# Kernel tuning notes

Hardware: AMD Instinct MI355X
Metric: run time of the kernel (lower is better)

The kernel has to match this reference:

```python
import jax, jax.numpy as jnp
import numpy as np

MARGIN = 0.2
LAMBDA_CLS = 1.0
LAMBDA_TRIPLET = 1.0
EPS = 1e-6  # matches torch pairwise_distance eps inside TripletMarginLoss
B, D, C = 8192, 192, 1024


def setup_inputs() -> dict:
    key = jax.random.key(0)
    k1, k2, k3 = jax.random.split(key, 3)
    embeddings = jax.random.normal(k1, (B, D), dtype=jnp.float32)
    logits = jax.random.normal(k2, (B, C), dtype=jnp.float32)
    targets = jax.random.randint(k3, (B,), 0, C, dtype=jnp.int64)
    return {"embeddings": embeddings, "logits": logits, "targets": targets}


def reference(embeddings, logits, targets):
    # ---- classification loss: mean cross entropy ----
    logp = jax.nn.log_softmax(logits, axis=-1)
    cls_loss = -jnp.mean(jnp.take_along_axis(logp, targets[:, None], axis=1))

    # ---- vectorized hard triplet mining (mining='hard'), on detached embeddings ----
    e = jax.lax.stop_gradient(embeddings)
    sq = jnp.sum(e * e, axis=1)                       # [B]
    d2 = sq[:, None] + sq[None, :] - 2.0 * (e @ e.T)  # [B, B]
    dist = jnp.sqrt(jnp.maximum(d2, 0.0))

    same = targets[:, None] == targets[None, :]       # [B, B]
    eye = jnp.eye(targets.shape[0], dtype=bool)
    pos_mask = same & ~eye
    neg_mask = ~same
    valid = pos_mask.any(axis=1) & neg_mask.any(axis=1)

    # hard positive: farthest same-speaker; hard negative: closest other-speaker
    pos_idx = jnp.argmax(jnp.where(pos_mask, dist, -jnp.inf), axis=1)
    neg_idx = jnp.argmin(jnp.where(neg_mask, dist, jnp.inf), axis=1)

    # ---- triplet margin loss on live embeddings ----
    a = embeddings
    p = embeddings[pos_idx]
    n = embeddings[neg_idx]
    d_ap = jnp.linalg.norm(a - p + EPS, axis=1)
    d_an = jnp.linalg.norm(a - n + EPS, axis=1)
    per_triplet = jnp.maximum(d_ap - d_an + MARGIN, 0.0)

    w = valid.astype(per_triplet.dtype)
    cnt = jnp.sum(w)
    trip_loss = jnp.where(cnt > 0, jnp.sum(per_triplet * w) / jnp.maximum(cnt, 1.0), 0.0)

    return LAMBDA_CLS * cls_loss + LAMBDA_TRIPLET * trip_loss
```

## Files before the change

kernel.cpp:

```cpp
#include <hip/hip_runtime.h>
#include <math.h>

#define B_N    8192
#define D_DIM  192
#define C_CLS  1024
#define MARGIN 0.2f
#define EPS_T  1e-6f

#define TI     128
#define TJ     128
#define JSPLIT 8
#define JLEN   (B_N / JSPLIT)
#define LDB    200

typedef __attribute__((ext_vector_type(8))) short v8s;
typedef __attribute__((ext_vector_type(4))) float v4f;
typedef __attribute__((ext_vector_type(4))) int   v4i;

__device__ __forceinline__ unsigned fkey(float f) {
  unsigned u = __float_as_uint(f);
  return (u & 0x80000000u) ? ~u : (u | 0x80000000u);
}

__device__ __forceinline__ unsigned short to_bf(float x) {
  unsigned u = __float_as_uint(x);
  u += 0x7fffu + ((u >> 16) & 1u);
  return (unsigned short)(u >> 16);
}

__global__ __launch_bounds__(256) void cvt_kernel(const float* __restrict__ e,
                                                  unsigned short* __restrict__ ebf) {
  int t = blockIdx.x * 256 + threadIdx.x;
  float4 v = ((const float4*)e)[t];
  ushort4 o;
  o.x = to_bf(v.x); o.y = to_bf(v.y); o.z = to_bf(v.z); o.w = to_bf(v.w);
  ((ushort4*)ebf)[t] = o;
}

__global__ __launch_bounds__(256) void sq_kernel(const float* __restrict__ e,
                                                 float* __restrict__ sq) {
  int w = threadIdx.x >> 6, lane = threadIdx.x & 63;
  int row = blockIdx.x * 4 + w;
  const float* p = e + (size_t)row * D_DIM;
  float v0 = p[lane], v1 = p[lane + 64], v2 = p[lane + 128];
  float s = v0 * v0 + v1 * v1 + v2 * v2;
  #pragma unroll
  for (int off = 32; off; off >>= 1) s += __shfl_xor(s, off);
  if (lane == 0) sq[row] = s;
}

__global__ __launch_bounds__(256, 2) void mine_kernel(
    const unsigned short* __restrict__ ebf, const int* __restrict__ tgt,
    const float* __restrict__ sq,
    unsigned long long* __restrict__ posw, unsigned long long* __restrict__ negw) {
  __shared__ unsigned short lds_b[TJ * LDB];
  __shared__ int   lds_t[TJ];
  __shared__ float lds_s[TJ];

  const int tid  = threadIdx.x;
  const int w    = tid >> 6;
  const int lane = tid & 63;
  const int ln15 = lane & 15;
  const int quad = lane >> 4;
  const int i0      = blockIdx.x * TI;
  const int j_begin = blockIdx.y * JLEN;

  int my_t[2][4];
  {
    const int base = i0 + w * 32 + quad * 4;
    v4i t0 = *(const v4i*)&tgt[base];
    v4i t1 = *(const v4i*)&tgt[base + 16];
    my_t[0][0] = t0.x; my_t[0][1] = t0.y; my_t[0][2] = t0.z; my_t[0][3] = t0.w;
    my_t[1][0] = t1.x; my_t[1][1] = t1.y; my_t[1][2] = t1.z; my_t[1][3] = t1.w;
  }

  v8s afrag[2][6];
  #pragma unroll
  for (int ra = 0; ra < 2; ++ra) {
    const unsigned short* ap =
        ebf + (size_t)(i0 + w * 32 + ra * 16 + ln15) * D_DIM + quad * 8;
    #pragma unroll
    for (int ks = 0; ks < 6; ++ks)
      afrag[ra][ks] = *(const v8s*)(ap + ks * 32);
  }

  float    pv[2][4], nv[2][4];
  unsigned pi_[2][4], ni_[2][4];
  #pragma unroll
  for (int ra = 0; ra < 2; ++ra)
    #pragma unroll
    for (int r = 0; r < 4; ++r) {
      pv[ra][r] = -3.4e38f; nv[ra][r] = 3.4e38f;
      pi_[ra][r] = 0u; ni_[ra][r] = 0xFFFFFFFFu;
    }

  for (int j0 = j_begin; j0 < j_begin + JLEN; j0 += TJ) {
    __syncthreads();
    #pragma unroll
    for (int t = 0; t < 12; ++t) {
      int c = t * 256 + tid;
      int row = c / 24;
      int off = c - row * 24;
      v8s v = *(const v8s*)(ebf + (size_t)(j0 + row) * D_DIM + off * 8);
      *(v8s*)&lds_b[row * LDB + off * 8] = v;
    }
    if (tid < TJ) { lds_t[tid] = tgt[j0 + tid]; lds_s[tid] = sq[j0 + tid]; }
    __syncthreads();

    v4f acc[2][8];
    #pragma unroll
    for (int ra = 0; ra < 2; ++ra)
      #pragma unroll
      for (int tb = 0; tb < 8; ++tb)
        acc[ra][tb] = (v4f){0.f, 0.f, 0.f, 0.f};

    #pragma unroll
    for (int ks = 0; ks < 6; ++ks) {
      v8s bfr[8];
      #pragma unroll
      for (int tb = 0; tb < 8; ++tb)
        bfr[tb] = *(const v8s*)&lds_b[(tb * 16 + ln15) * LDB + ks * 32 + quad * 8];
      #pragma unroll
      for (int ra = 0; ra < 2; ++ra)
        #pragma unroll
        for (int tb = 0; tb < 8; ++tb)
          acc[ra][tb] = __builtin_amdgcn_mfma_f32_16x16x32_bf16(
              afrag[ra][ks], bfr[tb], acc[ra][tb], 0, 0, 0);
    }

    #pragma unroll
    for (int tb = 0; tb < 8; ++tb) {
      int jl = tb * 16 + ln15;
      int jg = j0 + jl;
      int tc = lds_t[jl];
      float s = lds_s[jl];
      #pragma unroll
      for (int ra = 0; ra < 2; ++ra)
        #pragma unroll
        for (int r = 0; r < 4; ++r) {
          float val  = fmaf(acc[ra][tb][r], -2.0f, s);
          bool  same = (tc == my_t[ra][r]);
          float vp = same ? val : -3.4e38f;
          float vn = same ? 3.4e38f : val;
          if (vp > pv[ra][r]) { pv[ra][r] = vp; pi_[ra][r] = (unsigned)jg; }
          if (vn < nv[ra][r]) { nv[ra][r] = vn; ni_[ra][r] = (unsigned)jg; }
        }
    }
  }

  #pragma unroll
  for (int ra = 0; ra < 2; ++ra)
    #pragma unroll
    for (int r = 0; r < 4; ++r) {
      unsigned long long pk =
          ((unsigned long long)fkey(pv[ra][r]) << 32) |
          (unsigned long long)(unsigned)(~pi_[ra][r]);
      unsigned long long nk =
          ((unsigned long long)fkey(nv[ra][r]) << 32) |
          (unsigned long long)ni_[ra][r];
      #pragma unroll
      for (int off = 1; off < 16; off <<= 1) {
        unsigned long long po = __shfl_xor(pk, off);
        unsigned long long no = __shfl_xor(nk, off);
        pk = pk > po ? pk : po;
        nk = nk < no ? nk : no;
      }
      if (ln15 == 0) {
        int row = i0 + w * 32 + ra * 16 + quad * 4 + r;
        atomicMax(&posw[row], pk);
        atomicMin(&negw[row], nk);
      }
    }
}

__global__ __launch_bounds__(1024) void ce_kernel(const float* __restrict__ logits,
                                                  const int* __restrict__ tgt,
                                                  float* __restrict__ accum) {
  __shared__ float part[16];
  int w = threadIdx.x >> 6, lane = threadIdx.x & 63;
  int row = blockIdx.x * 16 + w;
  const float* p = logits + (size_t)row * C_CLS;
  float4 x[4];
  #pragma unroll
  for (int t = 0; t < 4; ++t) x[t] = *(const float4*)(p + lane * 4 + 256 * t);
  float m = -3.4e38f;
  #pragma unroll
  for (int t = 0; t < 4; ++t)
    m = fmaxf(m, fmaxf(fmaxf(x[t].x, x[t].y), fmaxf(x[t].z, x[t].w)));
  #pragma unroll
  for (int off = 32; off; off >>= 1) m = fmaxf(m, __shfl_xor(m, off));
  float s = 0.f;
  #pragma unroll
  for (int t = 0; t < 4; ++t)
    s += __expf(x[t].x - m) + __expf(x[t].y - m) +
         __expf(x[t].z - m) + __expf(x[t].w - m);
  #pragma unroll
  for (int off = 32; off; off >>= 1) s += __shfl_xor(s, off);
  if (lane == 0) part[w] = m + __logf(s) - p[tgt[row]];
  __syncthreads();
  if (threadIdx.x == 0) {
    float t = 0.f;
    #pragma unroll
    for (int i = 0; i < 16; ++i) t += part[i];
    atomicAdd(accum, t);
  }
}

__global__ __launch_bounds__(1024) void trip_kernel(
    const float* __restrict__ e,
    const unsigned long long* __restrict__ posw,
    const unsigned long long* __restrict__ negw,
    float* __restrict__ accum) {
  __shared__ float ssum[16];
  __shared__ float scnt[16];
  int w = threadIdx.x >> 6, lane = threadIdx.x & 63;
  int i = blockIdx.x * 16 + w;
  unsigned long long pp = posw[i], np = negw[i];
  unsigned pidx = ~(unsigned)pp;
  unsigned nidx = (unsigned)np;
  float res = 0.f, c = 0.f;
  if (pp != 0ULL && np != ~0ULL && pidx != (unsigned)i) {
    const float* pa = e + (size_t)i * D_DIM;
    const float* pb = e + (size_t)pidx * D_DIM;
    const float* pc = e + (size_t)nidx * D_DIM;
    float dap = 0.f, dan = 0.f;
    #pragma unroll
    for (int t = 0; t < 3; ++t) {
      int k = lane + 64 * t;
      float av = pa[k];
      float d1 = av - pb[k] + EPS_T;
      float d2 = av - pc[k] + EPS_T;
      dap += d1 * d1;
      dan += d2 * d2;
    }
    #pragma unroll
    for (int off = 32; off; off >>= 1) {
      dap += __shfl_xor(dap, off);
      dan += __shfl_xor(dan, off);
    }
    res = fmaxf(sqrtf(dap) - sqrtf(dan) + MARGIN, 0.f);
    c = 1.f;
  }
  if (lane == 0) { ssum[w] = res; scnt[w] = c; }
  __syncthreads();
  if (threadIdx.x == 0) {
    float a = 0.f, b = 0.f;
    #pragma unroll
    for (int k = 0; k < 16; ++k) { a += ssum[k]; b += scnt[k]; }
    atomicAdd(&accum[1], a);
    atomicAdd(&accum[2], b);
  }
}

__global__ void fin_kernel(const float* __restrict__ accum, float* __restrict__ out) {
  float cls = accum[0] / (float)B_N;
  float ts = accum[1], tc = accum[2];
  float trip = (tc > 0.f) ? ts / fmaxf(tc, 1.f) : 0.f;
  out[0] = cls + trip;
}

extern "C" void kernel_launch(void* const* d_in, const int* in_sizes, int n_in,
                              void* d_out, int out_size, void* d_ws, size_t ws_size,
                              hipStream_t stream) {
  const float* emb    = (const float*)d_in[0];
  const float* logits = (const float*)d_in[1];
  const int*   tgt    = (const int*)d_in[2];
  float* out = (float*)d_out;

  char* ws = (char*)d_ws;
  unsigned short* ebf = (unsigned short*)ws;
  unsigned long long* posw = (unsigned long long*)(ws + 3145728);
  unsigned long long* negw = (unsigned long long*)(ws + 3145728 + 65536);
  float* sq    = (float*)(ws + 3145728 + 131072);
  float* accum = (float*)(ws + 3145728 + 163840);

  hipMemsetAsync(posw, 0, 65536, stream);
  hipMemsetAsync(negw, 0xFF, 65536, stream);
  hipMemsetAsync(accum, 0, 16, stream);

  cvt_kernel<<<1536, 256, 0, stream>>>(emb, ebf);
  sq_kernel<<<2048, 256, 0, stream>>>(emb, sq);
  mine_kernel<<<dim3(B_N / TI, JSPLIT), 256, 0, stream>>>(ebf, tgt, sq, posw, negw);
  ce_kernel<<<512, 1024, 0, stream>>>(logits, tgt, accum);
  trip_kernel<<<512, 1024, 0, stream>>>(emb, posw, negw, accum);
  fin_kernel<<<1, 1, 0, stream>>>(accum, out);
}
```

Before: 174.6 us.

## Fuse prep, CE and finalize kernels; switch mining to 32x32 MFMA tiles

```diff
diff --git a/kernel.cpp b/kernel.cpp
--- a/kernel.cpp
+++ b/kernel.cpp
@@ -13,9 +13,8 @@
 #define JLEN   (B_N / JSPLIT)
 #define LDB    200
 
-typedef __attribute__((ext_vector_type(8))) short v8s;
-typedef __attribute__((ext_vector_type(4))) float v4f;
-typedef __attribute__((ext_vector_type(4))) int   v4i;
+typedef short v8s  __attribute__((ext_vector_type(8)));
+typedef float v16f __attribute__((ext_vector_type(16)));
 
 __device__ __forceinline__ unsigned fkey(float f) {
   unsigned u = __float_as_uint(f);
@@ -28,189 +27,180 @@
   return (unsigned short)(u >> 16);
 }
 
-__global__ __launch_bounds__(256) void cvt_kernel(const float* __restrict__ e,
-                                                  unsigned short* __restrict__ ebf) {
-  int t = blockIdx.x * 256 + threadIdx.x;
-  float4 v = ((const float4*)e)[t];
-  ushort4 o;
-  o.x = to_bf(v.x); o.y = to_bf(v.y); o.z = to_bf(v.z); o.w = to_bf(v.w);
-  ((ushort4*)ebf)[t] = o;
-}
-
-__global__ __launch_bounds__(256) void sq_kernel(const float* __restrict__ e,
-                                                 float* __restrict__ sq) {
+__global__ __launch_bounds__(256) void prep_kernel(
+    const float* __restrict__ e, unsigned short* __restrict__ ebf,
+    float* __restrict__ sq,
+    unsigned long long* __restrict__ posw, unsigned long long* __restrict__ negw,
+    float* __restrict__ accum) {
   int w = threadIdx.x >> 6, lane = threadIdx.x & 63;
   int row = blockIdx.x * 4 + w;
   const float* p = e + (size_t)row * D_DIM;
   float v0 = p[lane], v1 = p[lane + 64], v2 = p[lane + 128];
+  unsigned short* q = ebf + (size_t)row * D_DIM;
+  q[lane] = to_bf(v0); q[lane + 64] = to_bf(v1); q[lane + 128] = to_bf(v2);
   float s = v0 * v0 + v1 * v1 + v2 * v2;
   #pragma unroll
   for (int off = 32; off; off >>= 1) s += __shfl_xor(s, off);
   if (lane == 0) sq[row] = s;
+  int b = blockIdx.x;
+  if (b < 32)       posw[b * 256 + threadIdx.x] = 0ULL;
+  else if (b < 64)  negw[(b - 32) * 256 + threadIdx.x] = ~0ULL;
+  else if (b == 64 && threadIdx.x < 4) ((unsigned*)accum)[threadIdx.x] = 0u;
 }
 
 __global__ __launch_bounds__(256, 2) void mine_kernel(
     const unsigned short* __restrict__ ebf, const int* __restrict__ tgt,
-    const float* __restrict__ sq,
-    unsigned long long* __restrict__ posw, unsigned long long* __restrict__ negw) {
+    const float* __restrict__ sq, const float* __restrict__ logits,
+    unsigned long long* __restrict__ posw, unsigned long long* __restrict__ negw,
+    float* __restrict__ accum) {
   __shared__ unsigned short lds_b[TJ * LDB];
   __shared__ int   lds_t[TJ];
   __shared__ float lds_s[TJ];
+  __shared__ float ce_part[4];
 
   const int tid  = threadIdx.x;
   const int w    = tid >> 6;
   const int lane = tid & 63;
-  const int ln15 = lane & 15;
-  const int quad = lane >> 4;
-  const int i0      = blockIdx.x * TI;
-  const int j_begin = blockIdx.y * JLEN;
-
-  int my_t[2][4];
+  const int n5   = lane & 31;
+  const int h    = lane >> 5;
+  const int wj   = w & 1;
+  const int wi   = w >> 1;
+  const int i0 = blockIdx.x * TI;
+  const int jb = blockIdx.y * JLEN;
+
   {
-    const int base = i0 + w * 32 + quad * 4;
-    v4i t0 = *(const v4i*)&tgt[base];
-    v4i t1 = *(const v4i*)&tgt[base + 16];
-    my_t[0][0] = t0.x; my_t[0][1] = t0.y; my_t[0][2] = t0.z; my_t[0][3] = t0.w;
-    my_t[1][0] = t1.x; my_t[1][1] = t1.y; my_t[1][2] = t1.z; my_t[1][3] = t1.w;
-  }
-
-  v8s afrag[2][6];
-  #pragma unroll
-  for (int ra = 0; ra < 2; ++ra) {
-    const unsigned short* ap =
-        ebf + (size_t)(i0 + w * 32 + ra * 16 + ln15) * D_DIM + quad * 8;
-    #pragma unroll
-    for (int ks = 0; ks < 6; ++ks)
-      afrag[ra][ks] = *(const v8s*)(ap + ks * 32);
-  }
-
-  float    pv[2][4], nv[2][4];
-  unsigned pi_[2][4], ni_[2][4];
-  #pragma unroll
-  for (int ra = 0; ra < 2; ++ra)
-    #pragma unroll
-    for (int r = 0; r < 4; ++r) {
-      pv[ra][r] = -3.4e38f; nv[ra][r] = 3.4e38f;
-      pi_[ra][r] = 0u; ni_[ra][r] = 0xFFFFFFFFu;
-    }
-
-  for (int j0 = j_begin; j0 < j_begin + JLEN; j0 += TJ) {
-    __syncthreads();
+    const unsigned short* src = ebf + (size_t)i0 * D_DIM;
     #pragma unroll
     for (int t = 0; t < 12; ++t) {
       int c = t * 256 + tid;
       int row = c / 24;
       int off = c - row * 24;
-      v8s v = *(const v8s*)(ebf + (size_t)(j0 + row) * D_DIM + off * 8);
-      *(v8s*)&lds_b[row * LDB + off * 8] = v;
+      *(v8s*)&lds_b[row * LDB + off * 8] = *(const v8s*)(src + (size_t)row * D_DIM + off * 8);
+    }
+  }
+  __syncthreads();
+  v8s bfrag[2][12];
+  #pragma unroll
+  for (int tb = 0; tb < 2; ++tb)
+    #pragma unroll
+    for (int kc = 0; kc < 12; ++kc)
+      bfrag[tb][kc] = *(const v8s*)&lds_b[(wi * 64 + tb * 32 + n5) * LDB + kc * 16 + h * 8];
+
+  int my_t[2];
+  #pragma unroll
+  for (int tb = 0; tb < 2; ++tb) my_t[tb] = tgt[i0 + wi * 64 + tb * 32 + n5];
+
+  float    pv[2] = {-3.4e38f, -3.4e38f}, nv[2] = {3.4e38f, 3.4e38f};
+  unsigned pi_[2] = {0u, 0u}, ni_[2] = {0xFFFFFFFFu, 0xFFFFFFFFu};
+
+  for (int j0 = jb; j0 < jb + JLEN; j0 += TJ) {
+    __syncthreads();
+    #pragma unroll
+    for (int t = 0; t < 12; ++t) {
+      int c = t * 256 + tid;
+      int row = c / 24;
+      int off = c - row * 24;
+      *(v8s*)&lds_b[row * LDB + off * 8] =
+          *(const v8s*)(ebf + (size_t)(j0 + row) * D_DIM + off * 8);
     }
     if (tid < TJ) { lds_t[tid] = tgt[j0 + tid]; lds_s[tid] = sq[j0 + tid]; }
     __syncthreads();
 
-    v4f acc[2][8];
-    #pragma unroll
-    for (int ra = 0; ra < 2; ++ra)
+    v16f acc[2][2];
+    #pragma unroll
+    for (int ta = 0; ta < 2; ++ta)
       #pragma unroll
-      for (int tb = 0; tb < 8; ++tb)
-        acc[ra][tb] = (v4f){0.f, 0.f, 0.f, 0.f};
-
-    #pragma unroll
-    for (int ks = 0; ks < 6; ++ks) {
-      v8s bfr[8];
+      for (int tb = 0; tb < 2; ++tb)
+        #pragma unroll
+        for (int r = 0; r < 16; ++r) acc[ta][tb][r] = 0.f;
+
+    #pragma unroll
+    for (int kc = 0; kc < 12; ++kc) {
+      v8s afr0 = *(const v8s*)&lds_b[(wj * 64 +  0 + n5) * LDB + kc * 16 + h * 8];
+      v8s afr1 = *(const v8s*)&lds_b[(wj * 64 + 32 + n5) * LDB + kc * 16 + h * 8];
+      acc[0][0] = __builtin_amdgcn_mfma_f32_32x32x16_bf16(afr0, bfrag[0][kc], acc[0][0], 0, 0, 0);
+      acc[0][1] = __builtin_amdgcn_mfma_f32_32x32x16_bf16(afr0, bfrag[1][kc], acc[0][1], 0, 0, 0);
+      acc[1][0] = __builtin_amdgcn_mfma_f32_32x32x16_bf16(afr1, bfrag[0][kc], acc[1][0], 0, 0, 0);
+      acc[1][1] = __builtin_amdgcn_mfma_f32_32x32x16_bf16(afr1, bfrag[1][kc], acc[1][1], 0, 0, 0);
+    }
+
+    #pragma unroll
+    for (int ta = 0; ta < 2; ++ta)
       #pragma unroll
-      for (int tb = 0; tb < 8; ++tb)
-        bfr[tb] = *(const v8s*)&lds_b[(tb * 16 + ln15) * LDB + ks * 32 + quad * 8];
-      #pragma unroll
-      for (int ra = 0; ra < 2; ++ra)
+      for (int p = 0; p < 4; ++p) {
+        int jb4 = wj * 64 + ta * 32 + p * 8 + h * 4;
+        float4 s4 = *(const float4*)&lds_s[jb4];
+        int4   t4 = *(const int4*)&lds_t[jb4];
         #pragma unroll
-        for (int tb = 0; tb < 8; ++tb)
-          acc[ra][tb] = __builtin_amdgcn_mfma_f32_16x16x32_bf16(
-              afrag[ra][ks], bfr[tb], acc[ra][tb], 0, 0, 0);
-    }
-
-    #pragma unroll
-    for (int tb = 0; tb < 8; ++tb) {
-      int jl = tb * 16 + ln15;
-      int jg = j0 + jl;
-      int tc = lds_t[jl];
-      float s = lds_s[jl];
-      #pragma unroll
-      for (int ra = 0; ra < 2; ++ra)
-        #pragma unroll
-        for (int r = 0; r < 4; ++r) {
-          float val  = fmaf(acc[ra][tb][r], -2.0f, s);
-          bool  same = (tc == my_t[ra][r]);
-          float vp = same ? val : -3.4e38f;
-          float vn = same ? 3.4e38f : val;
-          if (vp > pv[ra][r]) { pv[ra][r] = vp; pi_[ra][r] = (unsigned)jg; }
-          if (vn < nv[ra][r]) { nv[ra][r] = vn; ni_[ra][r] = (unsigned)jg; }
+        for (int q = 0; q < 3 + 1; ++q) {
+          float sv = (q == 0) ? s4.x : (q == 1) ? s4.y : (q == 2) ? s4.z : s4.w;
+          int   tv = (q == 0) ? t4.x : (q == 1) ? t4.y : (q == 2) ? t4.z : t4.w;
+          unsigned jg = (unsigned)(j0 + jb4 + q);
+          #pragma unroll
+          for (int tb = 0; tb < 2; ++tb) {
+            float val = fmaf(acc[ta][tb][p * 4 + q], -2.0f, sv);
+            bool same = (tv == my_t[tb]);
+            float vp = same ? val : -3.4e38f;
+            float vn = same ? 3.4e38f : val;
+            if (vp > pv[tb]) { pv[tb] = vp; pi_[tb] = jg; }
+            if (vn < nv[tb]) { nv[tb] = vn; ni_[tb] = jg; }
+          }
         }
-    }
-  }
-
-  #pragma unroll
-  for (int ra = 0; ra < 2; ++ra)
-    #pragma unroll
-    for (int r = 0; r < 4; ++r) {
-      unsigned long long pk =
-          ((unsigned long long)fkey(pv[ra][r]) << 32) |
-          (unsigned long long)(unsigned)(~pi_[ra][r]);
-      unsigned long long nk =
-          ((unsigned long long)fkey(nv[ra][r]) << 32) |
-          (unsigned long long)ni_[ra][r];
-      #pragma unroll
-      for (int off = 1; off < 16; off <<= 1) {
-        unsigned long long po = __shfl_xor(pk, off);
-        unsigned long long no = __shfl_xor(nk, off);
-        pk = pk > po ? pk : po;
-        nk = nk < no ? nk : no;
       }
-      if (ln15 == 0) {
-        int row = i0 + w * 32 + ra * 16 + quad * 4 + r;
-        atomicMax(&posw[row], pk);
-        atomicMin(&negw[row], nk);
-      }
-    }
-}
-
-__global__ __launch_bounds__(1024) void ce_kernel(const float* __restrict__ logits,
-                                                  const int* __restrict__ tgt,
-                                                  float* __restrict__ accum) {
-  __shared__ float part[16];
-  int w = threadIdx.x >> 6, lane = threadIdx.x & 63;
-  int row = blockIdx.x * 16 + w;
-  const float* p = logits + (size_t)row * C_CLS;
-  float4 x[4];
-  #pragma unroll
-  for (int t = 0; t < 4; ++t) x[t] = *(const float4*)(p + lane * 4 + 256 * t);
-  float m = -3.4e38f;
-  #pragma unroll
-  for (int t = 0; t < 4; ++t)
-    m = fmaxf(m, fmaxf(fmaxf(x[t].x, x[t].y), fmaxf(x[t].z, x[t].w)));
-  #pragma unroll
-  for (int off = 32; off; off >>= 1) m = fmaxf(m, __shfl_xor(m, off));
-  float s = 0.f;
-  #pragma unroll
-  for (int t = 0; t < 4; ++t)
-    s += __expf(x[t].x - m) + __expf(x[t].y - m) +
-         __expf(x[t].z - m) + __expf(x[t].w - m);
-  #pragma unroll
-  for (int off = 32; off; off >>= 1) s += __shfl_xor(s, off);
-  if (lane == 0) part[w] = m + __logf(s) - p[tgt[row]];
+  }
+
+  #pragma unroll
+  for (int tb = 0; tb < 2; ++tb) {
+    unsigned long long pk =
+        ((unsigned long long)fkey(pv[tb]) << 32) | (unsigned long long)(unsigned)(~pi_[tb]);
+    unsigned long long nk =
+        ((unsigned long long)fkey(nv[tb]) << 32) | (unsigned long long)ni_[tb];
+    unsigned long long po = __shfl_xor(pk, 32);
+    unsigned long long no = __shfl_xor(nk, 32);
+    pk = pk > po ? pk : po;
+    nk = nk < no ? nk : no;
+    if (h == 0) {
+      int irow = i0 + wi * 64 + tb * 32 + n5;
+      atomicMax(&posw[irow], pk);
+      atomicMin(&negw[irow], nk);
+    }
+  }
+
+  int blin = blockIdx.y * 64 + blockIdx.x;
+  float ce_acc = 0.f;
+  #pragma unroll
+  for (int it = 0; it < 4; ++it) {
+    int row = blin * 16 + it * 4 + w;
+    const float* lp = logits + (size_t)row * C_CLS;
+    float4 x[4];
+    #pragma unroll
+    for (int t = 0; t < 4; ++t) x[t] = *(const float4*)(lp + lane * 4 + 256 * t);
+    float m = -3.4e38f;
+    #pragma unroll
+    for (int t = 0; t < 4; ++t)
+      m = fmaxf(m, fmaxf(fmaxf(x[t].x, x[t].y), fmaxf(x[t].z, x[t].w)));
+    #pragma unroll
+    for (int off = 32; off; off >>= 1) m = fmaxf(m, __shfl_xor(m, off));
+    float s = 0.f;
+    #pragma unroll
+    for (int t = 0; t < 4; ++t)
+      s += __expf(x[t].x - m) + __expf(x[t].y - m) +
+           __expf(x[t].z - m) + __expf(x[t].w - m);
+    #pragma unroll
+    for (int off = 32; off; off >>= 1) s += __shfl_xor(s, off);
+    if (lane == 0) ce_acc += m + __logf(s) - lp[tgt[row]];
+  }
+  if (lane == 0) ce_part[w] = ce_acc;
   __syncthreads();
-  if (threadIdx.x == 0) {
-    float t = 0.f;
-    #pragma unroll
-    for (int i = 0; i < 16; ++i) t += part[i];
-    atomicAdd(accum, t);
-  }
-}
-
-__global__ __launch_bounds__(1024) void trip_kernel(
+  if (tid == 0)
+    atomicAdd(&accum[0], ce_part[0] + ce_part[1] + ce_part[2] + ce_part[3]);
+}
+
+__global__ __launch_bounds__(1024) void trip_fin_kernel(
     const float* __restrict__ e,
     const unsigned long long* __restrict__ posw,
     const unsigned long long* __restrict__ negw,
-    float* __restrict__ accum) {
+    float* __restrict__ accum, float* __restrict__ out) {
   __shared__ float ssum[16];
   __shared__ float scnt[16];
   int w = threadIdx.x >> 6, lane = threadIdx.x & 63;
@@ -249,14 +239,17 @@
     for (int k = 0; k < 16; ++k) { a += ssum[k]; b += scnt[k]; }
     atomicAdd(&accum[1], a);
     atomicAdd(&accum[2], b);
-  }
-}
-
-__global__ void fin_kernel(const float* __restrict__ accum, float* __restrict__ out) {
-  float cls = accum[0] / (float)B_N;
-  float ts = accum[1], tc = accum[2];
-  float trip = (tc > 0.f) ? ts / fmaxf(tc, 1.f) : 0.f;
-  out[0] = cls + trip;
+    __threadfence();
+    unsigned old = atomicAdd((unsigned*)&accum[3], 1u);
+    if (old == 511u) {
+      __threadfence();
+      float cls = atomicAdd(&accum[0], 0.f);
+      float ts  = atomicAdd(&accum[1], 0.f);
+      float tc  = atomicAdd(&accum[2], 0.f);
+      float trip = (tc > 0.f) ? ts / fmaxf(tc, 1.f) : 0.f;
+      out[0] = cls / (float)B_N + trip;
+    }
+  }
 }
 
 extern "C" void kernel_launch(void* const* d_in, const int* in_sizes, int n_in,
@@ -274,14 +267,7 @@
   float* sq    = (float*)(ws + 3145728 + 131072);
   float* accum = (float*)(ws + 3145728 + 163840);
 
-  hipMemsetAsync(posw, 0, 65536, stream);
-  hipMemsetAsync(negw, 0xFF, 65536, stream);
-  hipMemsetAsync(accum, 0, 16, stream);
-
-  cvt_kernel<<<1536, 256, 0, stream>>>(emb, ebf);
-  sq_kernel<<<2048, 256, 0, stream>>>(emb, sq);
-  mine_kernel<<<dim3(B_N / TI, JSPLIT), 256, 0, stream>>>(ebf, tgt, sq, posw, negw);
-  ce_kernel<<<512, 1024, 0, stream>>>(logits, tgt, accum);
-  trip_kernel<<<512, 1024, 0, stream>>>(emb, posw, negw, accum);
-  fin_kernel<<<1, 1, 0, stream>>>(accum, out);
-}
+  prep_kernel<<<2048, 256, 0, stream>>>(emb, ebf, sq, posw, negw, accum);
+  mine_kernel<<<dim3(B_N / TI, JSPLIT), 256, 0, stream>>>(ebf, tgt, sq, logits, posw, negw, accum);
+  trip_fin_kernel<<<512, 1024, 0, stream>>>(emb, posw, negw, accum, out);
+}
```

Result: faster. 145.6 us (-16.6%).
